# Performance work log

Measured on AMD Instinct MI355X. Metric: run time of the kernel, lower is better.

Reference implementation:

```python
import jax, jax.numpy as jnp
import numpy as np

EMB = 768
HEADS = 12
DK = EMB // HEADS


def setup_inputs() -> dict:
    key = jax.random.key(0)
    ks = jax.random.split(key, 11)
    B, S = 2, 2048
    lim = 1.0 / np.sqrt(EMB)
    def lin(k):
        kw, kb = jax.random.split(k)
        W = jax.random.uniform(kw, (EMB, EMB), jnp.float32, -lim, lim)
        b = jax.random.uniform(kb, (EMB,), jnp.float32, -lim, lim)
        return W, b
    Wq, bq = lin(ks[0])
    Wk, bk = lin(ks[1])
    Wv, bv = lin(ks[2])
    Wo, bo = lin(ks[3])
    return {
        "query": jax.random.normal(ks[4], (B, S, EMB), jnp.float32),
        "key": jax.random.normal(ks[5], (B, S, EMB), jnp.float32),
        "value": jax.random.normal(ks[6], (B, S, EMB), jnp.float32),
        "Wq": Wq, "bq": bq, "Wk": Wk, "bk": bk,
        "Wv": Wv, "bv": bv, "Wo": Wo, "bo": bo,
    }


def reference(query, key, value, Wq, bq, Wk, bk, Wv, bv, Wo, bo):
    B, S, _ = query.shape
    # nn.Linear: x @ W^T + b, then split heads -> [B, H, S, d_k]
    def proj(x, W, b):
        return (x @ W.T + b).reshape(B, -1, HEADS, DK).transpose(0, 2, 1, 3)
    q = proj(query, Wq, bq)
    k = proj(key, Wk, bk)
    v = proj(value, Wv, bv)
    scale = 1.0 / jnp.sqrt(jnp.float32(DK))
    scores = jnp.einsum('bhqd,bhkd->bhqk', q, k) * scale  # [B,H,S,S]
    attn = jax.nn.softmax(scores, axis=-1)
    av = jnp.einsum('bhqk,bhkd->bhqd', attn, v)
    concat = av.transpose(0, 2, 1, 3).reshape(B, -1, EMB)
    return concat @ Wo.T + bo
```

## Files before the change

kernel.cpp:

```cpp
#include <hip/hip_runtime.h>
#include <hip/hip_bf16.h>

#define EMB 768
#define HEADS 12
#define DKV 64
#define BATCH 2
#define SEQ 2048
#define NTOK (BATCH*SEQ)

typedef float f32x4 __attribute__((ext_vector_type(4)));
typedef unsigned short u16;
typedef u16 u16x8 __attribute__((ext_vector_type(8)));
typedef u16 u16x4 __attribute__((ext_vector_type(4)));
typedef __bf16 bf16x8 __attribute__((ext_vector_type(8)));

__device__ __forceinline__ u16 f2bf(float f) {
  return __builtin_bit_cast(u16, (__bf16)f);
}
__device__ __forceinline__ float fexp2(float x) {
#if __has_builtin(__builtin_amdgcn_exp2f)
  return __builtin_amdgcn_exp2f(x);
#else
  return exp2f(x);
#endif
}
__device__ __forceinline__ f32x4 mfma16(u16x8 a, u16x8 b, f32x4 c) {
  return __builtin_amdgcn_mfma_f32_16x16x32_bf16(
      __builtin_bit_cast(bf16x8, a), __builtin_bit_cast(bf16x8, b), c, 0, 0, 0);
}

template<int MODE, bool AF32>
__device__ __forceinline__ void gemm_core(
    const void* __restrict__ Ap, const float* __restrict__ Bm,
    const float* __restrict__ bias, float ascale, float bscale,
    void* __restrict__ outp, u16* __restrict__ At, u16* __restrict__ Bt,
    int m0, int n0)
{
  const int t = threadIdx.x;
  const int w = t >> 6, lane = t & 63, lg = lane >> 4, lr = lane & 15;
  const int wr = w >> 1, wc = w & 1;
  const int tr = t >> 3, tsl = t & 7;

  f32x4 acc[2][4] = {};
  f32x4 raf[2][2];
  u16x8 rab[2];
  f32x4 rbf[4][2];

  auto STAGE_LOAD = [&](int kb) {
    #pragma unroll
    for (int q = 0; q < 2; ++q) {
      int row = q*32 + tr;
      if constexpr (AF32) {
        const float* p = (const float*)Ap + (size_t)(m0+row)*EMB + kb + tsl*8;
        raf[q][0] = *reinterpret_cast<const f32x4*>(p);
        raf[q][1] = *reinterpret_cast<const f32x4*>(p + 4);
      } else {
        rab[q] = *reinterpret_cast<const u16x8*>(
            (const u16*)Ap + (size_t)(m0+row)*EMB + kb + tsl*8);
      }
    }
    #pragma unroll
    for (int q = 0; q < 4; ++q) {
      int row = q*32 + tr;
      const float* p = Bm + (size_t)(n0+row)*EMB + kb + tsl*8;
      rbf[q][0] = *reinterpret_cast<const f32x4*>(p);
      rbf[q][1] = *reinterpret_cast<const f32x4*>(p + 4);
    }
  };

  auto STAGE_WRITE = [&](int bi) {
    #pragma unroll
    for (int q = 0; q < 2; ++q) {
      int row = q*32 + tr;
      u16x8 v;
      if constexpr (AF32) {
        #pragma unroll
        for (int j = 0; j < 4; ++j) {
          v[j]   = f2bf(raf[q][0][j] * ascale);
          v[4+j] = f2bf(raf[q][1][j] * ascale);
        }
      } else v = rab[q];
      *reinterpret_cast<u16x8*>(&At[bi*4096 + row*64 + ((tsl ^ (row & 7))*8)]) = v;
    }
    #pragma unroll
    for (int q = 0; q < 4; ++q) {
      int row = q*32 + tr;
      u16x8 v;
      #pragma unroll
      for (int j = 0; j < 4; ++j) {
        v[j]   = f2bf(rbf[q][0][j]);
        v[4+j] = f2bf(rbf[q][1][j]);
      }
      *reinterpret_cast<u16x8*>(&Bt[bi*8192 + row*64 + ((tsl ^ (row & 7))*8)]) = v;
    }
  };

  auto COMPUTE = [&](int bi) {
    u16x8 af[2][2], bfr[4][2];
    #pragma unroll
    for (int fm = 0; fm < 2; ++fm)
      #pragma unroll
      for (int kk = 0; kk < 2; ++kk) {
        int r = wr*32 + fm*16 + lr;
        int slot = (lg + 4*kk) ^ (r & 7);
        af[fm][kk] = *reinterpret_cast<const u16x8*>(&At[bi*4096 + r*64 + slot*8]);
      }
    #pragma unroll
    for (int fn = 0; fn < 4; ++fn)
      #pragma unroll
      for (int kk = 0; kk < 2; ++kk) {
        int r = wc*64 + fn*16 + lr;
        int slot = (lg + 4*kk) ^ (r & 7);
        bfr[fn][kk] = *reinterpret_cast<const u16x8*>(&Bt[bi*8192 + r*64 + slot*8]);
      }
    __builtin_amdgcn_s_setprio(1);
    #pragma unroll
    for (int fm = 0; fm < 2; ++fm)
      #pragma unroll
      for (int fn = 0; fn < 4; ++fn)
        #pragma unroll
        for (int kk = 0; kk < 2; ++kk)
          acc[fm][fn] = mfma16(af[fm][kk], bfr[fn][kk], acc[fm][fn]);
    __builtin_amdgcn_s_setprio(0);
  };

  STAGE_LOAD(0);
  STAGE_WRITE(0);
  __syncthreads();
  const int NSTEP = EMB/64;
  #pragma unroll
  for (int ts = 0; ts < NSTEP-1; ++ts) {
    STAGE_LOAD((ts+1)*64);
    COMPUTE(ts & 1);
    STAGE_WRITE((ts & 1) ^ 1);
    __syncthreads();
  }
  COMPUTE((NSTEP-1) & 1);

  #pragma unroll
  for (int fm = 0; fm < 2; ++fm)
    #pragma unroll
    for (int fn = 0; fn < 4; ++fn) {
      const int mb = m0 + wr*32 + fm*16 + lg*4;
      const int e  = n0 + wc*64 + fn*16 + lr;
      if constexpr (MODE == 2) {
        int bb = mb >> 11, sb = mb & 2047, h = e >> 6, d = e & 63;
        u16x4 o4;
        #pragma unroll
        for (int j = 0; j < 4; ++j) o4[j] = f2bf(acc[fm][fn][j] + bias[e]*bscale);
        *reinterpret_cast<u16x4*>(
            reinterpret_cast<u16*>(outp) + (((size_t)(bb*HEADS+h))*DKV + d)*SEQ + sb) = o4;
      } else {
        #pragma unroll
        for (int j = 0; j < 4; ++j) {
          int m = mb + j;
          float val = acc[fm][fn][j] + bias[e]*bscale;
          if constexpr (MODE == 0) {
            int bb = m >> 11, s = m & 2047, h = e >> 6, d = e & 63;
            reinterpret_cast<u16*>(outp)[(((size_t)(bb*HEADS+h))*SEQ + s)*DKV + d] = f2bf(val);
          } else {
            reinterpret_cast<float*>(outp)[(size_t)m*EMB + e] = val;
          }
        }
      }
    }
}

__global__ __launch_bounds__(256) void qkv_k(
    const float* __restrict__ Aq, const float* __restrict__ Ak, const float* __restrict__ Av,
    const float* __restrict__ Wq, const float* __restrict__ Wk, const float* __restrict__ Wv,
    const float* __restrict__ bq, const float* __restrict__ bk, const float* __restrict__ bv,
    u16* __restrict__ Qh, u16* __restrict__ Kh, u16* __restrict__ Vh, float csc)
{
  __shared__ __align__(16) u16 At[2*64*64];
  __shared__ __align__(16) u16 Bt[2*128*64];
  const int m0 = blockIdx.x*64, n0 = blockIdx.y*128;
  const int z = blockIdx.z;
  if (z == 0)
    gemm_core<0,true>(Aq, Wq, bq, csc, csc, Qh, At, Bt, m0, n0);
  else if (z == 1)
    gemm_core<0,true>(Ak, Wk, bk, 1.f, 1.f, Kh, At, Bt, m0, n0);
  else
    gemm_core<2,true>(Av, Wv, bv, 1.f, 1.f, Vh, At, Bt, m0, n0);
}

__global__ __launch_bounds__(256) void gemm_out_k(
    const u16* __restrict__ A, const float* __restrict__ Bm,
    const float* __restrict__ bias, float* __restrict__ outp)
{
  __shared__ __align__(16) u16 At[2*64*64];
  __shared__ __align__(16) u16 Bt[2*128*64];
  gemm_core<1,false>(A, Bm, bias, 1.f, 1.f, outp, At, Bt, blockIdx.x*64, blockIdx.y*128);
}

__global__ __launch_bounds__(256) void flash_attn_k(
    const u16* __restrict__ Q, const u16* __restrict__ K, const u16* __restrict__ VT,
    u16* __restrict__ av)
{
  __shared__ __align__(16) u16 Kt[2][64*64];
  __shared__ __align__(16) u16 Vt[2][64*64];
  __shared__ __align__(16) u16 Pt[4][16*64];

  const int t = threadIdx.x;
  const int w = t >> 6, lane = t & 63, lg = lane >> 4, lr = lane & 15;
  const int tr = t >> 3, tsl = t & 7;
  const int qb = blockIdx.x;
  const int bh = blockIdx.y;
  const u16* Qb = Q  + (size_t)bh*SEQ*DKV;
  const u16* Kb = K  + (size_t)bh*SEQ*DKV;
  const u16* Vb = VT + (size_t)bh*DKV*SEQ;

  const int qrow = qb*64 + w*16 + lr;
  u16x8 qf[2];
  qf[0] = *reinterpret_cast<const u16x8*>(Qb + (size_t)qrow*DKV + lg*8);
  qf[1] = *reinterpret_cast<const u16x8*>(Qb + (size_t)qrow*DKV + 32 + lg*8);

  f32x4 acc[4] = {};
  float mrun = -1e30f, lrun = 0.f;

  u16x8 ks[2], vs[2];
  auto LOADKV = [&](int kt0) {
    #pragma unroll
    for (int q = 0; q < 2; ++q) {
      int row = q*32 + tr;
      ks[q] = *reinterpret_cast<const u16x8*>(Kb + (size_t)(kt0+row)*DKV + tsl*8);
    }
    #pragma unroll
    for (int q = 0; q < 2; ++q) {
      int d = q*32 + tr;
      vs[q] = *reinterpret_cast<const u16x8*>(Vb + (size_t)d*SEQ + kt0 + tsl*8);
    }
  };

  const int NT = SEQ/64;
  LOADKV(0);
  {
    #pragma unroll
    for (int q = 0; q < 2; ++q) {
      int row = q*32 + tr;
      *reinterpret_cast<u16x8*>(&Kt[0][row*64 + ((tsl ^ (row & 7))*8)]) = ks[q];
    }
    #pragma unroll
    for (int q = 0; q < 2; ++q) {
      int d = q*32 + tr;
      *reinterpret_cast<u16x8*>(&Vt[0][d*64 + ((tsl ^ (d & 7))*8)]) = vs[q];
    }
  }
  __syncthreads();

  char* Pw = reinterpret_cast<char*>(&Pt[w][0]);

#define TILE(bi, kt)                                                          \
  do {                                                                        \
    if ((kt)+1 < NT) LOADKV(((kt)+1)*64);                                     \
    f32x4 s[4];                                                               \
    __builtin_amdgcn_s_setprio(1);                                            \
    _Pragma("unroll")                                                         \
    for (int fc = 0; fc < 4; ++fc) {                                          \
      f32x4 z = {};                                                           \
      _Pragma("unroll")                                                       \
      for (int kk = 0; kk < 2; ++kk) {                                        \
        int r = fc*16 + lr;                                                   \
        int slot = (lg + 4*kk) ^ (r & 7);                                     \
        u16x8 kf = *reinterpret_cast<const u16x8*>(&Kt[bi][r*64 + slot*8]);   \
        z = mfma16(kf, qf[kk], z);                                            \
      }                                                                       \
      s[fc] = z;                                                              \
    }                                                                         \
    __builtin_amdgcn_s_setprio(0);                                            \
    float a0 = fmaxf(fmaxf(s[0][0], s[0][1]), s[0][2]);                       \
    float a1 = fmaxf(fmaxf(s[0][3], s[1][0]), s[1][1]);                       \
    float a2 = fmaxf(fmaxf(s[1][2], s[1][3]), s[2][0]);                       \
    float a3 = fmaxf(fmaxf(s[2][1], s[2][2]), s[2][3]);                       \
    float a4 = fmaxf(fmaxf(s[3][0], s[3][1]), s[3][2]);                       \
    float pmax = fmaxf(fmaxf(fmaxf(a0, a1), a2),                              \
                       fmaxf(fmaxf(a3, a4), s[3][3]));                        \
    if (__any(pmax > mrun + 8.f)) {          \
      float pm = fmaxf(pmax, __shfl_xor(pmax, 16));                           \
      pm = fmaxf(pm, __shfl_xor(pm, 32));                                     \
      float mnew = fmaxf(mrun, pm);                                           \
      float corr = fexp2(mrun - mnew);                                        \
      mrun = mnew; lrun *= corr;                                              \
      _Pragma("unroll")                                                       \
      for (int fc = 0; fc < 4; ++fc)                                          \
        _Pragma("unroll")                                                     \
        for (int j = 0; j < 4; ++j)                                           \
          acc[fc][j] *= corr;                                                 \
    }                                                                         \
    float p[4][4], rs[4];                                                     \
    _Pragma("unroll")                                                         \
    for (int fc = 0; fc < 4; ++fc) {                                          \
      _Pragma("unroll")                                                       \
      for (int j = 0; j < 4; ++j) p[fc][j] = fexp2(s[fc][j] - mrun);          \
      rs[fc] = (p[fc][0] + p[fc][1]) + (p[fc][2] + p[fc][3]);                 \
    }                                                                         \
    lrun += (rs[0] + rs[1]) + (rs[2] + rs[3]);      \
    _Pragma("unroll")                                                         \
    for (int fc = 0; fc < 4; ++fc) {                                          \
      u16x4 q4;                                                               \
      _Pragma("unroll")                                                       \
      for (int j = 0; j < 4; ++j) q4[j] = f2bf(p[fc][j]);                     \
      *reinterpret_cast<u16x4*>(                                              \
          Pw + lr*128 + (((fc*4 + lg) ^ ((lr & 7) << 1))*8)) = q4;            \
    }                                                                         \
    asm volatile("s_waitcnt lgkmcnt(0)" ::: "memory");                        \
    __builtin_amdgcn_sched_barrier(0);                                        \
    __builtin_amdgcn_s_setprio(1);                                            \
    _Pragma("unroll")                                                         \
    for (int kk = 0; kk < 2; ++kk) {                                          \
      u16x8 pf = *reinterpret_cast<const u16x8*>(                             \
          Pw + lr*128 + (((kk*8 + lg*2) ^ ((lr & 7) << 1))*8));               \
      _Pragma("unroll")                                                       \
      for (int fc = 0; fc < 4; ++fc) {                                        \
        int rv = fc*16 + lr;                                                  \
        int slotv = (lg + 4*kk) ^ (rv & 7);                                   \
        u16x8 vf = *reinterpret_cast<const u16x8*>(&Vt[bi][rv*64 + slotv*8]); \
        acc[fc] = mfma16(vf, pf, acc[fc]);                                    \
      }                                                                       \
    }                                                                         \
    __builtin_amdgcn_s_setprio(0);                                            \
    if ((kt)+1 < NT) {                                                        \
      _Pragma("unroll")                                                       \
      for (int q = 0; q < 2; ++q) {                                           \
        int row = q*32 + tr;                                                  \
        *reinterpret_cast<u16x8*>(                                            \
            &Kt[(bi)^1][row*64 + ((tsl ^ (row & 7))*8)]) = ks[q];             \
      }                                                                       \
      _Pragma("unroll")                                                       \
      for (int q = 0; q < 2; ++q) {                                           \
        int d = q*32 + tr;                                                    \
        *reinterpret_cast<u16x8*>(                                            \
            &Vt[(bi)^1][d*64 + ((tsl ^ (d & 7))*8)]) = vs[q];                 \
      }                                                                       \
    }                                                                         \
    __syncthreads();                                                          \
  } while (0)

  for (int kt = 0; kt < NT; kt += 2) {
    TILE(0, kt);
    TILE(1, kt+1);
  }
#undef TILE

  float lt = lrun;
  lt += __shfl_xor(lt, 16);
  lt += __shfl_xor(lt, 32);
  const float inv = 1.0f / lt;

  const int b = bh / HEADS, h = bh % HEADS;
  #pragma unroll
  for (int fc = 0; fc < 4; ++fc) {
    u16x4 o4;
    #pragma unroll
    for (int j = 0; j < 4; ++j) o4[j] = f2bf(acc[fc][j] * inv);
    *reinterpret_cast<u16x4*>(
        av + ((size_t)(b*SEQ + qrow))*EMB + h*64 + fc*16 + lg*4) = o4;
  }
}

extern "C" void kernel_launch(void* const* d_in, const int* in_sizes, int n_in,
                              void* d_out, int out_size, void* d_ws, size_t ws_size,
                              hipStream_t stream) {
  const float* xq_f = (const float*)d_in[0];
  const float* xk_f = (const float*)d_in[1];
  const float* xv_f = (const float*)d_in[2];
  const float* Wq = (const float*)d_in[3];
  const float* bq = (const float*)d_in[4];
  const float* Wk = (const float*)d_in[5];
  const float* bk = (const float*)d_in[6];
  const float* Wv = (const float*)d_in[7];
  const float* bv = (const float*)d_in[8];
  const float* Wo = (const float*)d_in[9];
  const float* bo = (const float*)d_in[10];

  u16* Qh = (u16*)d_ws;
  u16* Kh = Qh + (size_t)NTOK*EMB;
  u16* Vh = Kh + (size_t)NTOK*EMB;
  u16* Xb = Vh + (size_t)NTOK*EMB;

  const float csc = 0.125f * 1.4426950408889634f;

  qkv_k<<<dim3(NTOK/64, EMB/128, 3), dim3(256), 0, stream>>>(
      xq_f, xk_f, xv_f, Wq, Wk, Wv, bq, bk, bv, Qh, Kh, Vh, csc);

  flash_attn_k<<<dim3(SEQ/64, BATCH*HEADS), dim3(256), 0, stream>>>(Qh, Kh, Vh, Xb);

  gemm_out_k<<<dim3(NTOK/64, EMB/128), dim3(256), 0, stream>>>(Xb, Wo, bo, (float*)d_out);
}
```

Baseline: 101.0 us.

## Software-pipeline flash attention QK and PV stages, shrink GEMM N-tile to 64

The attention loop is restructured so the QK^T MFMAs for the current key tile are issued together with the PV MFMAs for the previous tile. P is double-buffered per wave in shared memory so softmax exp work can overlap matrix-core work instead of serializing behind it. Separately, the projection and output GEMMs drop from 64x128 to 64x64 tiles, doubling the grid to improve CU occupancy and load balance. The cost is an extra barrier per attention iteration, more shared memory for P, and lower per-block data reuse in the GEMMs.

```diff
diff --git a/kernel.cpp b/kernel.cpp
--- a/kernel.cpp
+++ b/kernel.cpp
@@ -41,10 +41,10 @@
   const int wr = w >> 1, wc = w & 1;
   const int tr = t >> 3, tsl = t & 7;
 
-  f32x4 acc[2][4] = {};
+  f32x4 acc[2][2] = {};
   f32x4 raf[2][2];
   u16x8 rab[2];
-  f32x4 rbf[4][2];
+  f32x4 rbf[2][2];
 
   auto STAGE_LOAD = [&](int kb) {
     #pragma unroll
@@ -60,7 +60,7 @@
       }
     }
     #pragma unroll
-    for (int q = 0; q < 4; ++q) {
+    for (int q = 0; q < 2; ++q) {
       int row = q*32 + tr;
       const float* p = Bm + (size_t)(n0+row)*EMB + kb + tsl*8;
       rbf[q][0] = *reinterpret_cast<const f32x4*>(p);
@@ -83,7 +83,7 @@
       *reinterpret_cast<u16x8*>(&At[bi*4096 + row*64 + ((tsl ^ (row & 7))*8)]) = v;
     }
     #pragma unroll
-    for (int q = 0; q < 4; ++q) {
+    for (int q = 0; q < 2; ++q) {
       int row = q*32 + tr;
       u16x8 v;
       #pragma unroll
@@ -91,12 +91,12 @@
         v[j]   = f2bf(rbf[q][0][j]);
         v[4+j] = f2bf(rbf[q][1][j]);
       }
-      *reinterpret_cast<u16x8*>(&Bt[bi*8192 + row*64 + ((tsl ^ (row & 7))*8)]) = v;
+      *reinterpret_cast<u16x8*>(&Bt[bi*4096 + row*64 + ((tsl ^ (row & 7))*8)]) = v;
     }
   };
 
   auto COMPUTE = [&](int bi) {
-    u16x8 af[2][2], bfr[4][2];
+    u16x8 af[2][2], bfr[2][2];
     #pragma unroll
     for (int fm = 0; fm < 2; ++fm)
       #pragma unroll
@@ -106,18 +106,18 @@
         af[fm][kk] = *reinterpret_cast<const u16x8*>(&At[bi*4096 + r*64 + slot*8]);
       }
     #pragma unroll
-    for (int fn = 0; fn < 4; ++fn)
+    for (int fn = 0; fn < 2; ++fn)
       #pragma unroll
       for (int kk = 0; kk < 2; ++kk) {
-        int r = wc*64 + fn*16 + lr;
+        int r = wc*32 + fn*16 + lr;
         int slot = (lg + 4*kk) ^ (r & 7);
-        bfr[fn][kk] = *reinterpret_cast<const u16x8*>(&Bt[bi*8192 + r*64 + slot*8]);
+        bfr[fn][kk] = *reinterpret_cast<const u16x8*>(&Bt[bi*4096 + r*64 + slot*8]);
       }
     __builtin_amdgcn_s_setprio(1);
     #pragma unroll
     for (int fm = 0; fm < 2; ++fm)
       #pragma unroll
-      for (int fn = 0; fn < 4; ++fn)
+      for (int fn = 0; fn < 2; ++fn)
         #pragma unroll
         for (int kk = 0; kk < 2; ++kk)
           acc[fm][fn] = mfma16(af[fm][kk], bfr[fn][kk], acc[fm][fn]);
@@ -140,9 +140,9 @@
   #pragma unroll
   for (int fm = 0; fm < 2; ++fm)
     #pragma unroll
-    for (int fn = 0; fn < 4; ++fn) {
+    for (int fn = 0; fn < 2; ++fn) {
       const int mb = m0 + wr*32 + fm*16 + lg*4;
-      const int e  = n0 + wc*64 + fn*16 + lr;
+      const int e  = n0 + wc*32 + fn*16 + lr;
       if constexpr (MODE == 2) {
         int bb = mb >> 11, sb = mb & 2047, h = e >> 6, d = e & 63;
         u16x4 o4;
@@ -173,8 +173,8 @@
     u16* __restrict__ Qh, u16* __restrict__ Kh, u16* __restrict__ Vh, float csc)
 {
   __shared__ __align__(16) u16 At[2*64*64];
-  __shared__ __align__(16) u16 Bt[2*128*64];
-  const int m0 = blockIdx.x*64, n0 = blockIdx.y*128;
+  __shared__ __align__(16) u16 Bt[2*64*64];
+  const int m0 = blockIdx.x*64, n0 = blockIdx.y*64;
   const int z = blockIdx.z;
   if (z == 0)
     gemm_core<0,true>(Aq, Wq, bq, csc, csc, Qh, At, Bt, m0, n0);
@@ -189,8 +189,8 @@
     const float* __restrict__ bias, float* __restrict__ outp)
 {
   __shared__ __align__(16) u16 At[2*64*64];
-  __shared__ __align__(16) u16 Bt[2*128*64];
-  gemm_core<1,false>(A, Bm, bias, 1.f, 1.f, outp, At, Bt, blockIdx.x*64, blockIdx.y*128);
+  __shared__ __align__(16) u16 Bt[2*64*64];
+  gemm_core<1,false>(A, Bm, bias, 1.f, 1.f, outp, At, Bt, blockIdx.x*64, blockIdx.y*64);
 }
 
 __global__ __launch_bounds__(256) void flash_attn_k(
@@ -199,7 +199,7 @@
 {
   __shared__ __align__(16) u16 Kt[2][64*64];
   __shared__ __align__(16) u16 Vt[2][64*64];
-  __shared__ __align__(16) u16 Pt[4][16*64];
+  __shared__ __align__(16) u16 Pt[4][2][16*64];
 
   const int t = threadIdx.x;
   const int w = t >> 6, lane = t & 63, lg = lane >> 4, lr = lane & 15;
@@ -217,6 +217,7 @@
 
   f32x4 acc[4] = {};
   float mrun = -1e30f, lrun = 0.f;
+  f32x4 s[4];
 
   u16x8 ks[2], vs[2];
   auto LOADKV = [&](int kt0) {
@@ -233,28 +234,23 @@
   };
 
   const int NT = SEQ/64;
-  LOADKV(0);
-  {
-    #pragma unroll
-    for (int q = 0; q < 2; ++q) {
-      int row = q*32 + tr;
-      *reinterpret_cast<u16x8*>(&Kt[0][row*64 + ((tsl ^ (row & 7))*8)]) = ks[q];
-    }
-    #pragma unroll
-    for (int q = 0; q < 2; ++q) {
-      int d = q*32 + tr;
-      *reinterpret_cast<u16x8*>(&Vt[0][d*64 + ((tsl ^ (d & 7))*8)]) = vs[q];
-    }
-  }
-  __syncthreads();
-
-  char* Pw = reinterpret_cast<char*>(&Pt[w][0]);
-
-#define TILE(bi, kt)                                                          \
+
+#define WKV(bi)                                                               \
   do {                                                                        \
-    if ((kt)+1 < NT) LOADKV(((kt)+1)*64);                                     \
-    f32x4 s[4];                                                               \
-    __builtin_amdgcn_s_setprio(1);                                            \
+    _Pragma("unroll")                                                         \
+    for (int q = 0; q < 2; ++q) {                                             \
+      int row = q*32 + tr;                                                    \
+      *reinterpret_cast<u16x8*>(&Kt[bi][row*64 + ((tsl ^ (row & 7))*8)]) = ks[q]; \
+    }                                                                         \
+    _Pragma("unroll")                                                         \
+    for (int q = 0; q < 2; ++q) {                                             \
+      int d = q*32 + tr;                                                      \
+      *reinterpret_cast<u16x8*>(&Vt[bi][d*64 + ((tsl ^ (d & 7))*8)]) = vs[q]; \
+    }                                                                         \
+  } while (0)
+
+#define QK_MFMA(bi)                                                           \
+  do {                                                                        \
     _Pragma("unroll")                                                         \
     for (int fc = 0; fc < 4; ++fc) {                                          \
       f32x4 z = {};                                                           \
@@ -267,7 +263,27 @@
       }                                                                       \
       s[fc] = z;                                                              \
     }                                                                         \
-    __builtin_amdgcn_s_setprio(0);                                            \
+  } while (0)
+
+#define PV_MFMA(bi)                                                           \
+  do {                                                                        \
+    const char* Pr = reinterpret_cast<const char*>(&Pt[w][bi][0]);            \
+    _Pragma("unroll")                                                         \
+    for (int kk = 0; kk < 2; ++kk) {                                          \
+      u16x8 pf = *reinterpret_cast<const u16x8*>(                             \
+          Pr + lr*128 + (((kk*8 + lg*2) ^ ((lr & 7) << 1))*8));               \
+      _Pragma("unroll")                                                       \
+      for (int fc = 0; fc < 4; ++fc) {                                        \
+        int rv = fc*16 + lr;                                                  \
+        int slotv = (lg + 4*kk) ^ (rv & 7);                                   \
+        u16x8 vf = *reinterpret_cast<const u16x8*>(&Vt[bi][rv*64 + slotv*8]); \
+        acc[fc] = mfma16(vf, pf, acc[fc]);                                    \
+      }                                                                       \
+    }                                                                         \
+  } while (0)
+
+#define SOFTMAX_PW(bi)                                                        \
+  do {                                                                        \
     float a0 = fmaxf(fmaxf(s[0][0], s[0][1]), s[0][2]);                       \
     float a1 = fmaxf(fmaxf(s[0][3], s[1][0]), s[1][1]);                       \
     float a2 = fmaxf(fmaxf(s[1][2], s[1][3]), s[2][0]);                       \
@@ -287,61 +303,55 @@
         for (int j = 0; j < 4; ++j)                                           \
           acc[fc][j] *= corr;                                                 \
     }                                                                         \
-    float p[4][4], rs[4];                                                     \
+    float p[4][4], rsv[4];                                                    \
     _Pragma("unroll")                                                         \
     for (int fc = 0; fc < 4; ++fc) {                                          \
       _Pragma("unroll")                                                       \
       for (int j = 0; j < 4; ++j) p[fc][j] = fexp2(s[fc][j] - mrun);          \
-      rs[fc] = (p[fc][0] + p[fc][1]) + (p[fc][2] + p[fc][3]);                 \
-    }                                                                         \
-    lrun += (rs[0] + rs[1]) + (rs[2] + rs[3]);      \
+      rsv[fc] = (p[fc][0] + p[fc][1]) + (p[fc][2] + p[fc][3]);                \
+    }                                                                         \
+    lrun += (rsv[0] + rsv[1]) + (rsv[2] + rsv[3]);                            \
+    char* Pw_ = reinterpret_cast<char*>(&Pt[w][bi][0]);                       \
     _Pragma("unroll")                                                         \
     for (int fc = 0; fc < 4; ++fc) {                                          \
       u16x4 q4;                                                               \
       _Pragma("unroll")                                                       \
       for (int j = 0; j < 4; ++j) q4[j] = f2bf(p[fc][j]);                     \
       *reinterpret_cast<u16x4*>(                                              \
-          Pw + lr*128 + (((fc*4 + lg) ^ ((lr & 7) << 1))*8)) = q4;            \
-    }                                                                         \
-    asm volatile("s_waitcnt lgkmcnt(0)" ::: "memory");                        \
-    __builtin_amdgcn_sched_barrier(0);                                        \
+          Pw_ + lr*128 + (((fc*4 + lg) ^ ((lr & 7) << 1))*8)) = q4;           \
+    }                                                                         \
+  } while (0)
+
+#define ITER(bi, kt)                                                          \
+  do {                                                                        \
     __builtin_amdgcn_s_setprio(1);                                            \
-    _Pragma("unroll")                                                         \
-    for (int kk = 0; kk < 2; ++kk) {                                          \
-      u16x8 pf = *reinterpret_cast<const u16x8*>(                             \
-          Pw + lr*128 + (((kk*8 + lg*2) ^ ((lr & 7) << 1))*8));               \
-      _Pragma("unroll")                                                       \
-      for (int fc = 0; fc < 4; ++fc) {                                        \
-        int rv = fc*16 + lr;                                                  \
-        int slotv = (lg + 4*kk) ^ (rv & 7);                                   \
-        u16x8 vf = *reinterpret_cast<const u16x8*>(&Vt[bi][rv*64 + slotv*8]); \
-        acc[fc] = mfma16(vf, pf, acc[fc]);                                    \
-      }                                                                       \
-    }                                                                         \
+    QK_MFMA(bi);                                                              \
+    PV_MFMA(bi^1);                                                            \
     __builtin_amdgcn_s_setprio(0);                                            \
-    if ((kt)+1 < NT) {                                                        \
-      _Pragma("unroll")                                                       \
-      for (int q = 0; q < 2; ++q) {                                           \
-        int row = q*32 + tr;                                                  \
-        *reinterpret_cast<u16x8*>(                                            \
-            &Kt[(bi)^1][row*64 + ((tsl ^ (row & 7))*8)]) = ks[q];             \
-      }                                                                       \
-      _Pragma("unroll")                                                       \
-      for (int q = 0; q < 2; ++q) {                                           \
-        int d = q*32 + tr;                                                    \
-        *reinterpret_cast<u16x8*>(                                            \
-            &Vt[(bi)^1][d*64 + ((tsl ^ (d & 7))*8)]) = vs[q];                 \
-      }                                                                       \
-    }                                                                         \
-    __syncthreads();                                                          \
+    SOFTMAX_PW(bi);                                                           \
+    __syncthreads();                       \
+    if ((kt)+1 < NT) WKV(bi^1);                  \
+    __syncthreads();                                    \
+    if ((kt)+2 < NT) LOADKV(((kt)+2)*64);                                     \
   } while (0)
 
-  for (int kt = 0; kt < NT; kt += 2) {
-    TILE(0, kt);
-    TILE(1, kt+1);
+  LOADKV(0);
+  WKV(0);
+  __syncthreads();
+  LOADKV(64);
+  QK_MFMA(0);
+  SOFTMAX_PW(0);
+  WKV(1);
+  __syncthreads();
+  LOADKV(128);
+
+  for (int kt = 1; kt+1 < NT; kt += 2) {
+    ITER(1, kt);
+    ITER(0, kt+1);
   }
-#undef TILE
-
+  ITER(1, NT-1);
+
+  PV_MFMA(1);
   float lt = lrun;
   lt += __shfl_xor(lt, 16);
   lt += __shfl_xor(lt, 32);
@@ -356,6 +366,11 @@
     *reinterpret_cast<u16x4*>(
         av + ((size_t)(b*SEQ + qrow))*EMB + h*64 + fc*16 + lg*4) = o4;
   }
+#undef ITER
+#undef SOFTMAX_PW
+#undef PV_MFMA
+#undef QK_MFMA
+#undef WKV
 }
 
 extern "C" void kernel_launch(void* const* d_in, const int* in_sizes, int n_in,
@@ -380,10 +395,10 @@
 
   const float csc = 0.125f * 1.4426950408889634f;
 
-  qkv_k<<<dim3(NTOK/64, EMB/128, 3), dim3(256), 0, stream>>>(
+  qkv_k<<<dim3(NTOK/64, EMB/64, 3), dim3(256), 0, stream>>>(
       xq_f, xk_f, xv_f, Wq, Wk, Wv, bq, bk, bv, Qh, Kh, Vh, csc);
 
   flash_attn_k<<<dim3(SEQ/64, BATCH*HEADS), dim3(256), 0, stream>>>(Qh, Kh, Vh, Xb);
 
-  gemm_out_k<<<dim3(NTOK/64, EMB/128), dim3(256), 0, stream>>>(Xb, Wo, bo, (float*)d_out);
-}
+  gemm_out_k<<<dim3(NTOK/64, EMB/64), dim3(256), 0, stream>>>(Xb, Wo, bo, (float*)d_out);
+}
```

After: 101.3 us. No clear change (+0.3%).
